# Performance work log

Hardware: AMD Instinct MI355X
Metric: run time of the kernel (lower is better)

Reference implementation:

```python
import jax, jax.numpy as jnp
import numpy as np

EMBED = 768
HEADS = 12
HEAD_DIM = EMBED // HEADS
HIDDEN = 4 * EMBED
EPS = 1e-5


def _layernorm(x, g, b):
    mu = jnp.mean(x, axis=-1, keepdims=True)
    var = jnp.var(x, axis=-1, keepdims=True)
    return (x - mu) * jax.lax.rsqrt(var + EPS) * g + b


def setup_inputs() -> dict:
    key = jax.random.key(0)
    ks = jax.random.split(key, 12)
    s_e = 1.0 / np.sqrt(EMBED)
    s_h = 1.0 / np.sqrt(HIDDEN)
    return {
        "x": jax.random.normal(ks[0], (2, 2048, EMBED), dtype=jnp.float32),
        "ln1_g": jnp.ones((EMBED,), jnp.float32),
        "ln1_b": jnp.zeros((EMBED,), jnp.float32),
        "qkv_w": jax.random.uniform(ks[1], (EMBED, 3 * EMBED), jnp.float32, -s_e, s_e),
        "qkv_b": jax.random.uniform(ks[2], (3 * EMBED,), jnp.float32, -s_e, s_e),
        "proj_w": jax.random.uniform(ks[3], (EMBED, EMBED), jnp.float32, -s_e, s_e),
        "proj_b": jax.random.uniform(ks[4], (EMBED,), jnp.float32, -s_e, s_e),
        "ln2_g": jnp.ones((EMBED,), jnp.float32),
        "ln2_b": jnp.zeros((EMBED,), jnp.float32),
        "fc1_w": jax.random.uniform(ks[5], (EMBED, HIDDEN), jnp.float32, -s_e, s_e),
        "fc1_b": jax.random.uniform(ks[6], (HIDDEN,), jnp.float32, -s_e, s_e),
        "fc2_w": jax.random.uniform(ks[7], (HIDDEN, EMBED), jnp.float32, -s_h, s_h),
        "fc2_b": jax.random.uniform(ks[8], (EMBED,), jnp.float32, -s_h, s_h),
    }


def reference(x, ln1_g, ln1_b, qkv_w, qkv_b, proj_w, proj_b,
              ln2_g, ln2_b, fc1_w, fc1_b, fc2_w, fc2_b):
    B, L, C = x.shape
    scale = HEAD_DIM ** -0.5

    # --- attention sublayer (pre-LN) ---
    h = _layernorm(x, ln1_g, ln1_b)
    qkv = h @ qkv_w + qkv_b                       # [B, L, 3C]
    qkv = qkv.reshape(B, L, 3, HEADS, HEAD_DIM)
    q = jnp.transpose(qkv[:, :, 0], (0, 2, 1, 3))  # [B, H, L, D]
    k = jnp.transpose(qkv[:, :, 1], (0, 2, 1, 3))
    v = jnp.transpose(qkv[:, :, 2], (0, 2, 1, 3))
    attn = jnp.einsum('bhqd,bhkd->bhqk', q, k) * scale  # [B, H, L, L]
    attn = jax.nn.softmax(attn, axis=-1)
    out = jnp.einsum('bhqk,bhkd->bhqd', attn, v)  # [B, H, L, D]
    out = jnp.transpose(out, (0, 2, 1, 3)).reshape(B, L, C)
    x = x + (out @ proj_w + proj_b)

    # --- FFN sublayer (pre-LN) ---
    h = _layernorm(x, ln2_g, ln2_b)
    h = jax.nn.gelu(h @ fc1_w + fc1_b, approximate=False)
    x = x + (h @ fc2_w + fc2_b)
    return x
```

## Files before the change

### kernel.cpp

```cpp
#include <hip/hip_runtime.h>
#include <hip/hip_bf16.h>
#include <math.h>

#define EMBED   768
#define NHEADS  12
#define HD      64
#define HIDDEN  3072
#define SEQ     2048
#define BATCH   2
#define ROWS    (BATCH*SEQ)

#define QSCALE  0.1803368801111204f

typedef __bf16 bf16_t;
typedef __attribute__((ext_vector_type(8))) __bf16 bf16x8;
typedef __attribute__((ext_vector_type(4))) __bf16 bf16x4;
typedef __attribute__((ext_vector_type(4))) short s16x4;
typedef __attribute__((ext_vector_type(4))) float f32x4;

static __device__ __forceinline__ f32x4 mfma16(bf16x8 a, bf16x8 b, f32x4 c) {
  return __builtin_amdgcn_mfma_f32_16x16x32_bf16(a, b, c, 0, 0, 0);
}

static __device__ __forceinline__ f32x4 mfma16x16(bf16x4 a, bf16x4 b, f32x4 c) {
#if defined(__HIP_DEVICE_COMPILE__)
# if __has_builtin(__builtin_amdgcn_mfma_f32_16x16x16bf16_1k)
  s16x4 ai, bi;
  __builtin_memcpy(&ai, &a, 8);
  __builtin_memcpy(&bi, &b, 8);
  return __builtin_amdgcn_mfma_f32_16x16x16bf16_1k(ai, bi, c, 0, 0, 0);
# elif __has_builtin(__builtin_amdgcn_mfma_f32_16x16x16_bf16)
  return __builtin_amdgcn_mfma_f32_16x16x16_bf16(a, b, c, 0, 0, 0);
# else
  bf16x8 a8 = {a[0], a[1], a[2], a[3],
               (bf16_t)0.f, (bf16_t)0.f, (bf16_t)0.f, (bf16_t)0.f};
  bf16x8 b8 = {b[0], b[1], b[2], b[3],
               (bf16_t)0.f, (bf16_t)0.f, (bf16_t)0.f, (bf16_t)0.f};
  return mfma16(a8, b8, c);
# endif
#else
  (void)a; (void)b;
  return c;
#endif
}

#if defined(__HIP_DEVICE_COMPILE__) && __has_builtin(__builtin_amdgcn_exp2f)
static __device__ __forceinline__ float fast_exp2(float x) {
  return __builtin_amdgcn_exp2f(x);
}
#else
static __device__ __forceinline__ float fast_exp2(float x) { return exp2f(x); }
#endif

#if defined(__HIP_DEVICE_COMPILE__) && __has_builtin(__builtin_amdgcn_rcpf)
static __device__ __forceinline__ float fast_rcp(float x) {
  return __builtin_amdgcn_rcpf(x);
}
#else
static __device__ __forceinline__ float fast_rcp(float x) { return 1.0f / x; }
#endif

typedef __attribute__((address_space(1))) const void gas_void;
typedef __attribute__((address_space(3))) void las_void;
static __device__ __forceinline__ void gll16(const void* g, void* l) {
  __builtin_amdgcn_global_load_lds((gas_void*)g, (las_void*)l, 16, 0, 0);
}

__global__ __launch_bounds__(256) void prep_kernel(
    const float* __restrict__ w0, bf16_t* __restrict__ o0,
    const float* __restrict__ w1, bf16_t* __restrict__ o1,
    const float* __restrict__ w2, bf16_t* __restrict__ o2,
    const float* __restrict__ w3, bf16_t* __restrict__ o3,
    const float* __restrict__ x,  const float* __restrict__ g,
    const float* __restrict__ bt, bf16_t* __restrict__ lnout)
{
  __shared__ float tile[32][33];
  __shared__ float red[8];
  int lin = blockIdx.x;
  if (lin < 6912) {
    const float* in; bf16_t* out; int R, C, bx, by;
    if (lin < 1728)      { in = w0; out = o0; R = 768;  C = 2304; bx = lin % 72; by = lin / 72; }
    else if (lin < 2304) { in = w1; out = o1; R = 768;  C = 768;  lin -= 1728; bx = lin % 24; by = lin / 24; }
    else if (lin < 4608) { in = w2; out = o2; R = 768;  C = 3072; lin -= 2304; bx = lin % 96; by = lin / 96; }
    else                 { in = w3; out = o3; R = 3072; C = 768;  lin -= 4608; bx = lin % 24; by = lin / 24; }
    int c0 = bx * 32, r0 = by * 32;
    int tx = threadIdx.x & 31, ty = threadIdx.x >> 5;
    #pragma unroll
    for (int p = 0; p < 4; ++p) {
      int r = ty + p * 8;
      tile[r][tx] = in[(size_t)(r0 + r) * C + c0 + tx];
    }
    __syncthreads();
    #pragma unroll
    for (int p = 0; p < 4; ++p) {
      int cc = ty + p * 8;
      out[(size_t)(c0 + cc) * R + r0 + tx] = (bf16_t)tile[tx][cc];
    }
    return;
  }
  int row = lin - 6912;
  int tid = threadIdx.x;
  const float* xr = x + (size_t)row * EMBED;
  float v0 = xr[tid], v1 = xr[tid + 256], v2 = xr[tid + 512];
  float s  = v0 + v1 + v2;
  float s2 = v0*v0 + v1*v1 + v2*v2;
  #pragma unroll
  for (int o = 32; o >= 1; o >>= 1) {
    s  += __shfl_xor(s,  o, 64);
    s2 += __shfl_xor(s2, o, 64);
  }
  int wave = tid >> 6, lane = tid & 63;
  if (lane == 0) { red[wave] = s; red[wave + 4] = s2; }
  __syncthreads();
  s  = red[0] + red[1] + red[2] + red[3];
  s2 = red[4] + red[5] + red[6] + red[7];
  float mu  = s * (1.0f / EMBED);
  float var = s2 * (1.0f / EMBED) - mu * mu;
  float rs  = rsqrtf(var + 1e-5f);
  bf16_t* orow = lnout + (size_t)row * EMBED;
  orow[tid]       = (bf16_t)((v0 - mu) * rs * g[tid]       + bt[tid]);
  orow[tid + 256] = (bf16_t)((v1 - mu) * rs * g[tid + 256] + bt[tid + 256]);
  orow[tid + 512] = (bf16_t)((v2 - mu) * rs * g[tid + 512] + bt[tid + 512]);
}

__global__ __launch_bounds__(256) void ln_kernel(
    const float* __restrict__ x, const float* __restrict__ g,
    const float* __restrict__ bt, bf16_t* __restrict__ out)
{
  int row = blockIdx.x;
  int tid = threadIdx.x;
  const float* xr = x + (size_t)row * EMBED;
  float v0 = xr[tid], v1 = xr[tid + 256], v2 = xr[tid + 512];
  float s  = v0 + v1 + v2;
  float s2 = v0*v0 + v1*v1 + v2*v2;
  #pragma unroll
  for (int o = 32; o >= 1; o >>= 1) {
    s  += __shfl_xor(s,  o, 64);
    s2 += __shfl_xor(s2, o, 64);
  }
  __shared__ float red[8];
  int wave = tid >> 6, lane = tid & 63;
  if (lane == 0) { red[wave] = s; red[wave + 4] = s2; }
  __syncthreads();
  s  = red[0] + red[1] + red[2] + red[3];
  s2 = red[4] + red[5] + red[6] + red[7];
  float mu  = s * (1.0f / EMBED);
  float var = s2 * (1.0f / EMBED) - mu * mu;
  float rs  = rsqrtf(var + 1e-5f);
  bf16_t* orow = out + (size_t)row * EMBED;
  orow[tid]       = (bf16_t)((v0 - mu) * rs * g[tid]       + bt[tid]);
  orow[tid + 256] = (bf16_t)((v1 - mu) * rs * g[tid + 256] + bt[tid + 256]);
  orow[tid + 512] = (bf16_t)((v2 - mu) * rs * g[tid + 512] + bt[tid + 512]);
}

template<int MODE, int BN>
__global__ __launch_bounds__(256) void gemm_kernel(
    const bf16_t* __restrict__ A, const bf16_t* __restrict__ WT,
    const float* __restrict__ bias, const float* __restrict__ res,
    void* __restrict__ outp, bf16_t* __restrict__ vt, int N, int K)
{
  constexpr int JT = BN / 32;
  __shared__ bf16_t As[128 * 64];
  __shared__ bf16_t Bs[BN * 64];
  int tid = threadIdx.x;
  int lane = tid & 63, wave = tid >> 6;
  int l15 = lane & 15, quad = lane >> 4;
  int wm = wave >> 1, wn = wave & 1;

  int Nn = N / BN;
  int lin = blockIdx.x;
  int khalf = 0, k_lo = 0, k_hi = K;
  if (MODE == 4) { khalf = lin & 1; lin >>= 1; k_lo = khalf * (K / 2); k_hi = k_lo + K / 2; }
  int bm = (lin & 7) + 8 * ((lin >> 3) / Nn);
  int bn = (lin >> 3) % Nn;
  int m0 = bm * 128, n0 = bn * BN;

  f32x4 acc[4][JT];
  #pragma unroll
  for (int i = 0; i < 4; ++i)
    #pragma unroll
    for (int j = 0; j < JT; ++j)
      acc[i][j] = (f32x4){0.f, 0.f, 0.f, 0.f};

  int grow = lane >> 3;
  int gcol = ((lane & 7) ^ grow) * 8;
  const bf16_t* abase = A  + (size_t)(m0 + wave * 32 + grow) * K + gcol;
  const bf16_t* bbase = WT + (size_t)(n0 + wave * (BN / 4) + grow) * K + gcol;
  int swk = l15 & 7;

  for (int k0 = k_lo; k0 < k_hi; k0 += 64) {
    #pragma unroll
    for (int a = 0; a < 4; ++a)
      gll16(abase + (size_t)a * 8 * K + k0, &As[(wave * 32 + a * 8) * 64]);
    #pragma unroll
    for (int a = 0; a < BN / 32; ++a)
      gll16(bbase + (size_t)a * 8 * K + k0, &Bs[(wave * (BN / 4) + a * 8) * 64]);
    __syncthreads();

    #pragma unroll
    for (int g = 0; g < 2; ++g) {
      bf16x8 af[4], bfr[JT];
      #pragma unroll
      for (int i = 0; i < 4; ++i)
        af[i] = *(const bf16x8*)
            &As[(wm * 64 + i * 16 + l15) * 64 + (((g * 4 + quad) ^ swk) * 8)];
      #pragma unroll
      for (int j = 0; j < JT; ++j)
        bfr[j] = *(const bf16x8*)
            &Bs[(wn * (BN / 2) + j * 16 + l15) * 64 + (((g * 4 + quad) ^ swk) * 8)];
      #pragma unroll
      for (int i = 0; i < 4; ++i)
        #pragma unroll
        for (int j = 0; j < JT; ++j)
          acc[i][j] = mfma16(af[i], bfr[j], acc[i][j]);
    }
    __syncthreads();
  }

  #pragma unroll
  for (int i = 0; i < 4; ++i) {
    int mbase = m0 + wm * 64 + i * 16 + quad * 4;
    #pragma unroll
    for (int j = 0; j < JT; ++j) {
      int n = n0 + wn * (BN / 2) + j * 16 + l15;
      float bn_ = (MODE == 4 && khalf != 0) ? 0.f : bias[n];
      if (MODE == 3 && n >= 1536) {
        int dcol = n - 1536;
        int hh = dcol >> 6, dd = dcol & 63;
        int bsel = mbase >> 11, l = mbase & 2047;
        union { bf16_t b4[4]; uint2 u; } pk;
        #pragma unroll
        for (int r = 0; r < 4; ++r)
          pk.b4[r] = (bf16_t)(acc[i][j][r] + bn_);
        *(uint2*)&vt[(((size_t)bsel * NHEADS + hh) * HD + dd) * SEQ + l] = pk.u;
        continue;
      }
      #pragma unroll
      for (int r = 0; r < 4; ++r) {
        size_t idx = (size_t)(mbase + r) * N + n;
        float v = acc[i][j][r] + bn_;
        if (MODE == 1) {
          float e = fast_exp2(fminf(v * (2.3020807f + 0.10293776f * v * v), 120.f));
          v = v * e * fast_rcp(e + 1.0f);
        }
        if (MODE == 3 && n < 768) v *= QSCALE;
        if (MODE == 2) {
          v += res[idx];
          ((float*)outp)[idx] = v;
        } else if (MODE == 4) {
          atomicAdd((float*)outp + idx, v);
        } else {
          ((bf16_t*)outp)[idx] = (bf16_t)v;
        }
      }
    }
  }
}

__global__ __launch_bounds__(256, 3) void attn_kernel(
    const bf16_t* __restrict__ qkv, const bf16_t* __restrict__ vt,
    bf16_t* __restrict__ attnout)
{
  __attribute__((aligned(16))) __shared__ bf16_t smem[4 * 4096];
  __shared__ float dsumf[4][64];

  int qt = blockIdx.x, h = blockIdx.y, b = blockIdx.z;
  int tid = threadIdx.x;
  int wave = tid >> 6, lane = tid & 63;
  int l15 = lane & 15, quad = lane >> 4;
  int q0 = qt * 64;
  int bh = b * NHEADS + h;

  bf16_t* wbase = smem + wave * 4096;

  bf16x8 bq[4][2];
  #pragma unroll
  for (int qi = 0; qi < 4; ++qi) {
    const bf16_t* qrow = qkv + (size_t)(b * SEQ + q0 + qi * 16 + l15) * 2304
                             + h * HD + quad * 8;
    bq[qi][0] = *(const bf16x8*)qrow;
    bq[qi][1] = *(const bf16x8*)(qrow + 32);
  }
  __asm__ volatile("s_waitcnt vmcnt(0)" ::: "memory");

  f32x4 accO[4][4];
  #pragma unroll
  for (int qi = 0; qi < 4; ++qi)
    #pragma unroll
    for (int t2 = 0; t2 < 4; ++t2)
      accO[qi][t2] = (f32x4){0.f, 0.f, 0.f, 0.f};
  float lpart[4] = {};

  int krow_l = lane >> 3;
  int kchunk = ((lane & 7) ^ krow_l) * 8;
  const bf16_t* ksrc0 = qkv + (size_t)(b * SEQ + wave * 16 + krow_l) * 2304
                            + 768 + h * HD + kchunk;
  int vrow_l = lane >> 1;
  int vchunk = (lane & 1) * 8;
  const bf16_t* vsrc0 = vt + ((size_t)bh * HD + vrow_l) * SEQ + wave * 16 + vchunk;

  constexpr int NIT = SEQ / 64;

  {
    bf16_t* kb = wbase;
    bf16_t* vb = wbase + 1024;
    #pragma unroll
    for (int p = 0; p < 2; ++p) {
      gll16(ksrc0 + (size_t)(p * 8) * 2304, kb + p * 512);
      gll16(vsrc0 + (size_t)(p * 32) * SEQ, vb + p * 512);
    }
  }

  int cb = 0;
  for (int it = 0; it < NIT; ++it) {
    {
      int kvn = ((it + 1) & (NIT - 1)) * 64;
      const bf16_t* ks = ksrc0 + (size_t)kvn * 2304;
      const bf16_t* vs = vsrc0 + kvn;
      bf16_t* kb = wbase + (cb ^ 1) * 2048;
      bf16_t* vb = kb + 1024;
      #pragma unroll
      for (int p = 0; p < 2; ++p) {
        gll16(ks + (size_t)(p * 8) * 2304, kb + p * 512);
        gll16(vs + (size_t)(p * 32) * SEQ, vb + p * 512);
      }
    }
    __asm__ volatile("s_waitcnt vmcnt(4)" ::: "memory");

    const bf16_t* kb = wbase + cb * 2048;
    const bf16_t* vb = kb + 1024;

    bf16x8 ak[2];
    #pragma unroll
    for (int f = 0; f < 2; ++f)
      ak[f] = *(const bf16x8*)
          &kb[l15 * 64 + (((f * 4 + quad) ^ (l15 & 7)) * 8)];

    bf16x4 bv[4];
    #pragma unroll
    for (int t2 = 0; t2 < 4; ++t2)
      bv[t2] = *(const bf16x4*)&vb[(t2 * 16 + l15) * 16 + quad * 4];

    #pragma unroll
    for (int qi = 0; qi < 4; ++qi) {
      f32x4 s = (f32x4){0.f, 0.f, 0.f, 0.f};
      s = mfma16(ak[0], bq[qi][0], s);
      s = mfma16(ak[1], bq[qi][1], s);
      bf16x4 ap;
      float ls = 0.f;
      #pragma unroll
      for (int r = 0; r < 4; ++r) {
        float pv = fast_exp2(s[r]);
        ls += pv;
        ap[r] = (bf16_t)pv;
      }
      lpart[qi] += ls;
      #pragma unroll
      for (int t2 = 0; t2 < 4; ++t2)
        accO[qi][t2] = mfma16x16(ap, bv[t2], accO[qi][t2]);
    }
    cb ^= 1;
  }

  #pragma unroll
  for (int qi = 0; qi < 4; ++qi) {
    float l = lpart[qi];
    l += __shfl_xor(l, 16, 64);
    l += __shfl_xor(l, 32, 64);
    if (quad == 0) dsumf[wave][qi * 16 + l15] = l;
  }
  __syncthreads();

  float* slabf = (float*)smem;

  for (int pass = 0; pass < 2; ++pass) {
    #pragma unroll
    for (int qi2 = 0; qi2 < 2; ++qi2) {
      int qi = pass * 2 + qi2;
      #pragma unroll
      for (int t2 = 0; t2 < 4; ++t2)
        #pragma unroll
        for (int r = 0; r < 4; ++r)
          slabf[wave * 2048 + (qi2 * 16 + quad * 4 + r) * 64 + t2 * 16 + l15]
              = accO[qi][t2][r];
    }
    __syncthreads();
    int row = tid >> 3;
    int d0 = (tid & 7) * 8;
    f32x4 o0 = (f32x4){0.f,0.f,0.f,0.f}, o1 = (f32x4){0.f,0.f,0.f,0.f};
    #pragma unroll
    for (int sw = 0; sw < 4; ++sw) {
      o0 += *(const f32x4*)&slabf[sw * 2048 + row * 64 + d0];
      o1 += *(const f32x4*)&slabf[sw * 2048 + row * 64 + d0 + 4];
    }
    int q_abs = pass * 32 + row;
    float den = dsumf[0][q_abs] + dsumf[1][q_abs] + dsumf[2][q_abs] + dsumf[3][q_abs];
    float inv = 1.0f / den;
    bf16_t ob[8];
    #pragma unroll
    for (int j = 0; j < 4; ++j) {
      ob[j]     = (bf16_t)(o0[j] * inv);
      ob[j + 4] = (bf16_t)(o1[j] * inv);
    }
    *(uint4*)&attnout[(size_t)(b * SEQ + q0 + q_abs) * EMBED + h * HD + d0]
        = *(const uint4*)ob;
    if (pass == 0) __syncthreads();
  }
}

extern "C" void kernel_launch(void* const* d_in, const int* in_sizes, int n_in,
                              void* d_out, int out_size, void* d_ws, size_t ws_size,
                              hipStream_t stream) {
  (void)in_sizes; (void)n_in; (void)out_size; (void)ws_size;
  const float* x      = (const float*)d_in[0];
  const float* ln1_g  = (const float*)d_in[1];
  const float* ln1_b  = (const float*)d_in[2];
  const float* qkv_w  = (const float*)d_in[3];
  const float* qkv_b  = (const float*)d_in[4];
  const float* proj_w = (const float*)d_in[5];
  const float* proj_b = (const float*)d_in[6];
  const float* ln2_g  = (const float*)d_in[7];
  const float* ln2_b  = (const float*)d_in[8];
  const float* fc1_w  = (const float*)d_in[9];
  const float* fc1_b  = (const float*)d_in[10];
  const float* fc2_w  = (const float*)d_in[11];
  const float* fc2_b  = (const float*)d_in[12];
  float* out = (float*)d_out;

  char* p = (char*)d_ws;
  bf16_t* wqkvT  = (bf16_t*)p; p += (size_t)2304 * 768 * 2;
  bf16_t* wprojT = (bf16_t*)p; p += (size_t)768 * 768 * 2;
  bf16_t* wfc1T  = (bf16_t*)p; p += (size_t)3072 * 768 * 2;
  bf16_t* wfc2T  = (bf16_t*)p; p += (size_t)768 * 3072 * 2;
  bf16_t* hbuf   = (bf16_t*)p; p += (size_t)ROWS * 768 * 2;
  bf16_t* qkv    = (bf16_t*)p;
  bf16_t* hid    = (bf16_t*)p; p += (size_t)ROWS * 3072 * 2;
  bf16_t* vt     = (bf16_t*)p; p += (size_t)BATCH * NHEADS * HD * SEQ * 2;
  bf16_t* attno  = (bf16_t*)p; p += (size_t)ROWS * 768 * 2;

  prep_kernel<<<6912 + ROWS, 256, 0, stream>>>(
      qkv_w, wqkvT, proj_w, wprojT, fc1_w, wfc1T, fc2_w, wfc2T,
      x, ln1_g, ln1_b, hbuf);

  gemm_kernel<3,128><<<32 * (2304/128), 256, 0, stream>>>(
      hbuf, wqkvT, qkv_b, nullptr, qkv, vt, 2304, 768);
  attn_kernel<<<dim3(SEQ/64, NHEADS, BATCH), 256, 0, stream>>>(qkv, vt, attno);
  gemm_kernel<2,64><<<32 * (768/64), 256, 0, stream>>>(
      attno, wprojT, proj_b, x, out, nullptr, 768, 768);

  ln_kernel<<<ROWS, 256, 0, stream>>>(out, ln2_g, ln2_b, hbuf);
  gemm_kernel<1,128><<<32 * (3072/128), 256, 0, stream>>>(
      hbuf, wfc1T, fc1_b, nullptr, hid, nullptr, 3072, 768);
  gemm_kernel<4,64><<<2 * 32 * (768/64), 256, 0, stream>>>(
      hid, wfc2T, fc2_b, nullptr, out, nullptr, 768, 3072);
}
```

Measured before the change: 265.0 us.

## Process two KV tiles per iteration with 16x16x32 MFMA and MFMA row-sums

Restructures the attention inner loop to handle two 64-key tiles per iteration, so that the P·V product uses the wider 16x16x32 bf16 MFMA in place of two 16x16x16 MFMAs. The softmax denominator is now accumulated by an MFMA against a vector of ones, replacing the scalar adds and cross-lane shuffles. Staging moves to a triple buffer, loading two tiles ahead with a new V-tile swizzle to avoid LDS bank conflicts. The trade-offs are more shared memory per block, which may lower occupancy, and a full vmcnt(0) wait that could expose load latency.

Result: faster. 259.2 us (-2.2%).

```diff
diff --git a/kernel.cpp b/kernel.cpp
--- a/kernel.cpp
+++ b/kernel.cpp
@@ -15,33 +15,10 @@
 typedef __bf16 bf16_t;
 typedef __attribute__((ext_vector_type(8))) __bf16 bf16x8;
 typedef __attribute__((ext_vector_type(4))) __bf16 bf16x4;
-typedef __attribute__((ext_vector_type(4))) short s16x4;
 typedef __attribute__((ext_vector_type(4))) float f32x4;
 
 static __device__ __forceinline__ f32x4 mfma16(bf16x8 a, bf16x8 b, f32x4 c) {
   return __builtin_amdgcn_mfma_f32_16x16x32_bf16(a, b, c, 0, 0, 0);
-}
-
-static __device__ __forceinline__ f32x4 mfma16x16(bf16x4 a, bf16x4 b, f32x4 c) {
-#if defined(__HIP_DEVICE_COMPILE__)
-# if __has_builtin(__builtin_amdgcn_mfma_f32_16x16x16bf16_1k)
-  s16x4 ai, bi;
-  __builtin_memcpy(&ai, &a, 8);
-  __builtin_memcpy(&bi, &b, 8);
-  return __builtin_amdgcn_mfma_f32_16x16x16bf16_1k(ai, bi, c, 0, 0, 0);
-# elif __has_builtin(__builtin_amdgcn_mfma_f32_16x16x16_bf16)
-  return __builtin_amdgcn_mfma_f32_16x16x16_bf16(a, b, c, 0, 0, 0);
-# else
-  bf16x8 a8 = {a[0], a[1], a[2], a[3],
-               (bf16_t)0.f, (bf16_t)0.f, (bf16_t)0.f, (bf16_t)0.f};
-  bf16x8 b8 = {b[0], b[1], b[2], b[3],
-               (bf16_t)0.f, (bf16_t)0.f, (bf16_t)0.f, (bf16_t)0.f};
-  return mfma16(a8, b8, c);
-# endif
-#else
-  (void)a; (void)b;
-  return c;
-#endif
 }
 
 #if defined(__HIP_DEVICE_COMPILE__) && __has_builtin(__builtin_amdgcn_exp2f)
@@ -261,7 +238,7 @@
     const bf16_t* __restrict__ qkv, const bf16_t* __restrict__ vt,
     bf16_t* __restrict__ attnout)
 {
-  __attribute__((aligned(16))) __shared__ bf16_t smem[4 * 4096];
+  __attribute__((aligned(16))) __shared__ bf16_t smem[4 * 3 * 2048];
   __shared__ float dsumf[4][64];
 
   int qt = blockIdx.x, h = blockIdx.y, b = blockIdx.z;
@@ -271,7 +248,7 @@
   int q0 = qt * 64;
   int bh = b * NHEADS + h;
 
-  bf16_t* wbase = smem + wave * 4096;
+  bf16_t* wbase = smem + wave * 3 * 2048;
 
   bf16x8 bq[4][2];
   #pragma unroll
@@ -284,90 +261,107 @@
   __asm__ volatile("s_waitcnt vmcnt(0)" ::: "memory");
 
   f32x4 accO[4][4];
-  #pragma unroll
-  for (int qi = 0; qi < 4; ++qi)
+  f32x4 accL[4];
+  #pragma unroll
+  for (int qi = 0; qi < 4; ++qi) {
+    accL[qi] = (f32x4){0.f, 0.f, 0.f, 0.f};
     #pragma unroll
     for (int t2 = 0; t2 < 4; ++t2)
       accO[qi][t2] = (f32x4){0.f, 0.f, 0.f, 0.f};
-  float lpart[4] = {};
+  }
+
+  bf16x8 ones;
+  #pragma unroll
+  for (int r = 0; r < 8; ++r) ones[r] = (bf16_t)1.0f;
 
   int krow_l = lane >> 3;
   int kchunk = ((lane & 7) ^ krow_l) * 8;
   const bf16_t* ksrc0 = qkv + (size_t)(b * SEQ + wave * 16 + krow_l) * 2304
                             + 768 + h * HD + kchunk;
   int vrow_l = lane >> 1;
-  int vchunk = (lane & 1) * 8;
+  int vchunk = ((lane & 1) ^ ((vrow_l >> 2) & 1)) * 8;
   const bf16_t* vsrc0 = vt + ((size_t)bh * HD + vrow_l) * SEQ + wave * 16 + vchunk;
 
   constexpr int NIT = SEQ / 64;
 
-  {
-    bf16_t* kb = wbase;
-    bf16_t* vb = wbase + 1024;
+  auto stage = [&](int t) {
+    bf16_t* kb = wbase + (t % 3) * 2048;
+    bf16_t* vb = kb + 1024;
+    const bf16_t* ks = ksrc0 + (size_t)(t * 64) * 2304;
+    const bf16_t* vs = vsrc0 + t * 64;
     #pragma unroll
     for (int p = 0; p < 2; ++p) {
-      gll16(ksrc0 + (size_t)(p * 8) * 2304, kb + p * 512);
-      gll16(vsrc0 + (size_t)(p * 32) * SEQ, vb + p * 512);
-    }
-  }
-
-  int cb = 0;
-  for (int it = 0; it < NIT; ++it) {
-    {
-      int kvn = ((it + 1) & (NIT - 1)) * 64;
-      const bf16_t* ks = ksrc0 + (size_t)kvn * 2304;
-      const bf16_t* vs = vsrc0 + kvn;
-      bf16_t* kb = wbase + (cb ^ 1) * 2048;
-      bf16_t* vb = kb + 1024;
-      #pragma unroll
-      for (int p = 0; p < 2; ++p) {
-        gll16(ks + (size_t)(p * 8) * 2304, kb + p * 512);
-        gll16(vs + (size_t)(p * 32) * SEQ, vb + p * 512);
+      gll16(ks + (size_t)(p * 8) * 2304, kb + p * 512);
+      gll16(vs + (size_t)(p * 32) * SEQ, vb + p * 512);
+    }
+  };
+
+  stage(0);
+  stage(1);
+
+  int vphys = (((quad >> 1) ^ ((l15 >> 2) & 1)) * 8) + (quad & 1) * 4;
+
+  for (int p = 0; p < NIT / 2; ++p) {
+    int ta = 2 * p, tb = 2 * p + 1;
+    __asm__ volatile("s_waitcnt vmcnt(0)" ::: "memory");
+
+    const bf16_t* kba = wbase + (ta % 3) * 2048;
+    const bf16_t* vba = kba + 1024;
+    const bf16_t* kbb = wbase + (tb % 3) * 2048;
+    const bf16_t* vbb = kbb + 1024;
+
+    bf16x8 aka[2], akb[2];
+    #pragma unroll
+    for (int f = 0; f < 2; ++f) {
+      int koff = (((f * 4 + quad) ^ (l15 & 7)) * 8);
+      aka[f] = *(const bf16x8*)&kba[l15 * 64 + koff];
+      akb[f] = *(const bf16x8*)&kbb[l15 * 64 + koff];
+    }
+
+    bf16x8 bv8[4];
+    #pragma unroll
+    for (int t2 = 0; t2 < 4; ++t2) {
+      bf16x4 lo = *(const bf16x4*)&vba[(t2 * 16 + l15) * 16 + vphys];
+      bf16x4 hi = *(const bf16x4*)&vbb[(t2 * 16 + l15) * 16 + vphys];
+      bf16x8 c;
+      #pragma unroll
+      for (int r = 0; r < 4; ++r) { c[r] = lo[r]; c[r + 4] = hi[r]; }
+      bv8[t2] = c;
+    }
+
+    __asm__ volatile("s_waitcnt lgkmcnt(0)" ::: "memory");
+    if (p < NIT / 2 - 1) {
+      stage(2 * p + 2);
+      stage(2 * p + 3);
+    }
+
+    #pragma unroll
+    for (int qi = 0; qi < 4; ++qi) {
+      f32x4 sa = (f32x4){0.f, 0.f, 0.f, 0.f};
+      sa = mfma16(aka[0], bq[qi][0], sa);
+      sa = mfma16(aka[1], bq[qi][1], sa);
+      f32x4 sb = (f32x4){0.f, 0.f, 0.f, 0.f};
+      sb = mfma16(akb[0], bq[qi][0], sb);
+      sb = mfma16(akb[1], bq[qi][1], sb);
+      bf16x8 ap;
+      #pragma unroll
+      for (int r = 0; r < 4; ++r) {
+        ap[r]     = (bf16_t)fast_exp2(sa[r]);
+        ap[r + 4] = (bf16_t)fast_exp2(sb[r]);
       }
-    }
-    __asm__ volatile("s_waitcnt vmcnt(4)" ::: "memory");
-
-    const bf16_t* kb = wbase + cb * 2048;
-    const bf16_t* vb = kb + 1024;
-
-    bf16x8 ak[2];
-    #pragma unroll
-    for (int f = 0; f < 2; ++f)
-      ak[f] = *(const bf16x8*)
-          &kb[l15 * 64 + (((f * 4 + quad) ^ (l15 & 7)) * 8)];
-
-    bf16x4 bv[4];
-    #pragma unroll
-    for (int t2 = 0; t2 < 4; ++t2)
-      bv[t2] = *(const bf16x4*)&vb[(t2 * 16 + l15) * 16 + quad * 4];
-
-    #pragma unroll
-    for (int qi = 0; qi < 4; ++qi) {
-      f32x4 s = (f32x4){0.f, 0.f, 0.f, 0.f};
-      s = mfma16(ak[0], bq[qi][0], s);
-      s = mfma16(ak[1], bq[qi][1], s);
-      bf16x4 ap;
-      float ls = 0.f;
-      #pragma unroll
-      for (int r = 0; r < 4; ++r) {
-        float pv = fast_exp2(s[r]);
-        ls += pv;
-        ap[r] = (bf16_t)pv;
-      }
-      lpart[qi] += ls;
+      accL[qi] = mfma16(ap, ones, accL[qi]);
       #pragma unroll
       for (int t2 = 0; t2 < 4; ++t2)
-        accO[qi][t2] = mfma16x16(ap, bv[t2], accO[qi][t2]);
-    }
-    cb ^= 1;
-  }
-
-  #pragma unroll
-  for (int qi = 0; qi < 4; ++qi) {
-    float l = lpart[qi];
-    l += __shfl_xor(l, 16, 64);
-    l += __shfl_xor(l, 32, 64);
-    if (quad == 0) dsumf[wave][qi * 16 + l15] = l;
+        accO[qi][t2] = mfma16(ap, bv8[t2], accO[qi][t2]);
+    }
+  }
+
+  if (l15 == 0) {
+    #pragma unroll
+    for (int qi = 0; qi < 4; ++qi)
+      #pragma unroll
+      for (int r = 0; r < 4; ++r)
+        dsumf[wave][qi * 16 + quad * 4 + r] = accL[qi][r];
   }
   __syncthreads();
 
```
